# Kernel optimization log

Measured on AMD Instinct MI355X. Metric: run time of the kernel, lower is better.

Reference implementation:

```python
import jax, jax.numpy as jnp
import numpy as np

SCALE = float(1 << 15)
PREEMPH = 0.97
FRAME_LEN = 400
FRAME_SHIFT = 160
FFT_SIZE = 512
N_RFFT = FFT_SIZE // 2 + 1  # 257
EPS = float(np.finfo(np.float32).eps)


def _mel_scale(f):
    return 1127.0 * np.log(1.0 + f / 700.0)


def _get_mel_banks(num_bins=80, window_length_padded=512, sample_freq=16000.0,
                   low_freq=20.0, high_freq=0.0):
    # Kaldi-style triangular mel banks (vtln_warp=1.0 -> no warp)
    num_fft_bins = window_length_padded // 2  # 256
    nyquist = 0.5 * sample_freq
    if high_freq <= 0.0:
        high_freq = nyquist + high_freq  # 8000.0
    fft_bin_width = sample_freq / window_length_padded
    mel_low = _mel_scale(low_freq)
    mel_high = _mel_scale(high_freq)
    mel_delta = (mel_high - mel_low) / (num_bins + 1)
    bins = np.arange(num_bins, dtype=np.float64)[:, None]
    left = mel_low + bins * mel_delta
    center = left + mel_delta
    right = center + mel_delta
    mel_freqs = _mel_scale(fft_bin_width * np.arange(num_fft_bins, dtype=np.float64))[None, :]
    up = (mel_freqs - left) / (center - left)
    down = (right - mel_freqs) / (right - center)
    banks = np.maximum(0.0, np.minimum(up, down))  # [80, 256]
    return banks.astype(np.float32)


def _buffers():
    # Hamming window, periodic=False: 0.54 - 0.46*cos(2*pi*n/(N-1))
    n = np.arange(FRAME_LEN, dtype=np.float64)
    window = (0.54 - 0.46 * np.cos(2.0 * np.pi * n / (FRAME_LEN - 1))).astype(np.float32)
    mel = _get_mel_banks()  # [80, 256]
    mel_padded = np.pad(mel, ((0, 0), (0, 1)))  # pad one zero column -> [80, 257]
    mel_filters = mel_padded.T.copy()  # [257, 80]
    k = np.arange(N_RFFT, dtype=np.float64)
    t = np.arange(FFT_SIZE, dtype=np.float64)
    angles = 2.0 * np.pi * k[:, None] * t[None, :] / FFT_SIZE
    dft_cos = np.cos(angles).astype(np.float32)  # [257, 512]
    dft_sin = np.sin(angles).astype(np.float32)  # [257, 512]
    return window, mel_filters, dft_cos, dft_sin


def setup_inputs() -> dict:
    key = jax.random.key(0)
    waveforms = jax.random.normal(key, (32, 1, 480000), dtype=jnp.float32)
    window, mel_filters, dft_cos, dft_sin = _buffers()
    return {
        "waveforms": waveforms,
        "window": jnp.asarray(window),
        "mel_filters": jnp.asarray(mel_filters),
        "dft_cos": jnp.asarray(dft_cos),
        "dft_sin": jnp.asarray(dft_sin),
    }


def reference(waveforms, window, mel_filters, dft_cos, dft_sin):
    signal = waveforms[:, 0, :] * SCALE  # [B, T]
    T = signal.shape[-1]
    n_frames = (T - FRAME_LEN) // FRAME_SHIFT + 1
    # strided framing (equivalent to conv1d with identity kernel, stride=160)
    idx = jnp.arange(n_frames)[:, None] * FRAME_SHIFT + jnp.arange(FRAME_LEN)[None, :]
    frames = signal[:, idx]  # [B, F, 400]
    frames = frames - jnp.mean(frames, axis=2, keepdims=True)
    # pre-emphasis with replicate-padded previous sample
    prev = jnp.concatenate([frames[..., :1], frames[..., :-1]], axis=-1)
    frames = (frames - PREEMPH * prev) * window  # windowing fused
    frames = jnp.pad(frames, ((0, 0), (0, 0), (0, FFT_SIZE - FRAME_LEN)))  # [B, F, 512]
    real = jnp.matmul(frames, dft_cos.T)  # [B, F, 257]
    imag = jnp.matmul(frames, dft_sin.T)
    spectrum = real * real + imag * imag  # power spectrum
    mel = jnp.matmul(spectrum, mel_filters)  # [B, F, 80]
    mel = jnp.log(jnp.maximum(mel, EPS))
    return mel - jnp.mean(mel, axis=1, keepdims=True)
```

## Files before the change

kernel.cpp:

```cpp
#include <hip/hip_runtime.h>

#define BATCH     32
#define T_SAMP    480000
#define NFRAMES   2998
#define KLEN      400
#define KF        256
#define NMEL      80
#define EPS_F     1.1920928955078125e-07f
#define SCALE2    1073741824.0f
#define SPLIT_S   2048.0f
#define SPLIT_INV 4.8828125e-4f
#define MTE       132
#define NPART     16

typedef _Float16 f16x8 __attribute__((ext_vector_type(8)));
typedef float    f32x4 __attribute__((ext_vector_type(4)));

__global__ __launch_bounds__(256) void FbankWrapper_14285061226526_kernel(float* mpart)
{
    int i = blockIdx.x * 256 + threadIdx.x;
    if (i < NPART * BATCH * NMEL) mpart[i] = 0.f;
}

__global__ __launch_bounds__(256) void k_prep(const float* __restrict__ melf,
                                              const float* __restrict__ dcos,
                                              const float* __restrict__ dsin,
                                              int* __restrict__ loE, int* __restrict__ hiE,
                                              int* __restrict__ loO, int* __restrict__ hiO,
                                              float* __restrict__ melfTe,
                                              float* __restrict__ melfTo,
                                              _Float16* __restrict__ Bhe, _Float16* __restrict__ Ble,
                                              _Float16* __restrict__ Bho, _Float16* __restrict__ Blo)
{
    const int bid = blockIdx.x;
    const int tid = threadIdx.x;

    if (bid < 80) {
        __shared__ int sE0, sE1, sO0, sO1;
        if (tid == 0) { sE0 = 999; sE1 = 0; sO0 = 999; sO1 = 0; }
        __syncthreads();
        const int m = bid;
        if (tid < 129) {
            int bin = (tid == 0) ? 0 : (tid == 128) ? 256 : 2 * tid;
            float w = melf[(size_t)bin * NMEL + m];
            melfTe[(size_t)m * MTE + tid] = w;
            if (w > 0.f) { atomicMin(&sE0, tid); atomicMax(&sE1, tid + 1); }
        }
        if (tid < 128) {
            float w = melf[(size_t)(2 * tid + 1) * NMEL + m];
            melfTo[(size_t)m * MTE + tid] = w;
            if (w > 0.f) { atomicMin(&sO0, tid); atomicMax(&sO1, tid + 1); }
        }
        if (tid == 0) {
            melfTe[(size_t)m * MTE + 129] = 0.f;
            melfTe[(size_t)m * MTE + 130] = 0.f;
            melfTe[(size_t)m * MTE + 131] = 0.f;
            melfTo[(size_t)m * MTE + 128] = 0.f;
            melfTo[(size_t)m * MTE + 129] = 0.f;
            melfTo[(size_t)m * MTE + 130] = 0.f;
            melfTo[(size_t)m * MTE + 131] = 0.f;
        }
        __syncthreads();
        if (tid == 0) { loE[m] = sE0; hiE[m] = sE1; loO[m] = sO0; hiO[m] = sO1; }
        return;
    }

    int id = (bid - 80) * 256 + tid;
    if (id >= 16384) return;
    int g  = id >> 13;
    int r  = id & 8191;
    int ch = r >> 8;
    int c  = r & 255;
    int k  = ch * 8;
    int bin; int sn;
    if (g == 0) { bin = (c == 0) ? 0 : (c == 1) ? 256 : 2 * (c >> 1); sn = (c >= 2) && (c & 1); }
    else        { bin = 2 * (c >> 1) + 1;                             sn = c & 1; }
    const float* src = (sn ? dsin : dcos) + (size_t)bin * 512 + k;
    f16x8 hv, lv;
    #pragma unroll
    for (int j = 0; j < 8; ++j) {
        float v = src[j];
        _Float16 h = (_Float16)v;
        hv[j] = h;
        lv[j] = (_Float16)((v - (float)h) * SPLIT_S);
    }
    size_t off = ((size_t)ch * 256 + c) * 8;
    *(f16x8*)((g ? Bho : Bhe) + off) = hv;
    *(f16x8*)((g ? Blo : Ble) + off) = lv;
}

__device__ inline void y8_compute(const float* __restrict__ sig,
                                  const float* __restrict__ window,
                                  int k0, float mean, float ys[8])
{
    float4 x0 = *(const float4*)(sig + k0);
    float4 x1 = *(const float4*)(sig + k0 + 4);
    float4 w0 = *(const float4*)(window + k0);
    float4 w1 = *(const float4*)(window + k0 + 4);
    float xm1 = (k0 > 0) ? sig[k0 - 1] : x0.x;
    float xs[8] = {x0.x, x0.y, x0.z, x0.w, x1.x, x1.y, x1.z, x1.w};
    float wv[8] = {w0.x, w0.y, w0.z, w0.w, w1.x, w1.y, w1.z, w1.w};
    #pragma unroll
    for (int j = 0; j < 8; ++j) {
        float xp = (j == 0) ? xm1 : xs[j - 1];
        ys[j] = (xs[j] - 0.97f * xp - 0.03f * mean) * wv[j];
    }
}

__device__ inline void split_store(_Float16* dh, _Float16* dl, const float ys[8])
{
    f16x8 hv, lv;
    #pragma unroll
    for (int j = 0; j < 8; ++j) {
        _Float16 h = (_Float16)ys[j];
        hv[j] = h;
        lv[j] = (_Float16)((ys[j] - (float)h) * SPLIT_S);
    }
    *(f16x8*)dh = hv;
    *(f16x8*)dl = lv;
}

__global__ __launch_bounds__(512, 4) void k_main_pre(const float* __restrict__ wav,
                                                     const float* __restrict__ window,
                                                     const float* __restrict__ melfTe,
                                                     const float* __restrict__ melfTo,
                                                     const int* __restrict__ loE,
                                                     const int* __restrict__ hiE,
                                                     const int* __restrict__ loO,
                                                     const int* __restrict__ hiO,
                                                     const _Float16* __restrict__ Bhe,
                                                     const _Float16* __restrict__ Ble,
                                                     const _Float16* __restrict__ Bho,
                                                     const _Float16* __restrict__ Blo,
                                                     float* __restrict__ out,
                                                     float* __restrict__ mpart)
{
    __shared__ __align__(16) _Float16 Aeh[32][264];
    __shared__ __align__(16) _Float16 Ael[32][264];
    __shared__ __align__(16) _Float16 Aoh[32][168];
    __shared__ __align__(16) _Float16 Aol[32][168];
    __shared__ __align__(16) float    Sp[32][132];

    const int tid  = threadIdx.x;
    const int lane = tid & 63;
    const int wid  = tid >> 6;
    const int tile = blockIdx.x;

    {
        int fr = tid >> 4, og = tid & 15;
        int fb = tile * 32 + fr;
        int b  = fb / NFRAMES;
        int f  = fb - b * NFRAMES;
        const float* sig = wav + (size_t)b * T_SAMP + (size_t)f * 160;

        float s = 0.f;
        #pragma unroll
        for (int i = 0; i < 4; ++i) {
            int k0 = og * 8 + 128 * i;
            if (k0 < KLEN) {
                float4 x0 = *(const float4*)(sig + k0);
                float4 x1 = *(const float4*)(sig + k0 + 4);
                s += x0.x + x0.y + x0.z + x0.w + x1.x + x1.y + x1.z + x1.w;
            }
        }
        s += __shfl_xor(s, 1);
        s += __shfl_xor(s, 2);
        s += __shfl_xor(s, 4);
        s += __shfl_xor(s, 8);
        float mean = s * (1.0f / (float)KLEN);

        #pragma unroll
        for (int t2 = 0; t2 < 2; ++t2) {
            int c  = og + 16 * t2;
            int k0 = c * 8;
            float ys[8];
            y8_compute(sig, window, k0, mean, ys);
            if (c < 18) {
                float yb[8], ye[8], yo[8];
                y8_compute(sig, window, k0 + 256, mean, yb);
                #pragma unroll
                for (int j = 0; j < 8; ++j) { ye[j] = ys[j] + yb[j]; yo[j] = ys[j] - yb[j]; }
                split_store(&Aeh[fr][k0], &Ael[fr][k0], ye);
                split_store(&Aoh[fr][k0], &Aol[fr][k0], yo);
            } else {
                split_store(&Aeh[fr][k0], &Ael[fr][k0], ys);
                if (k0 < 160)
                    split_store(&Aoh[fr][k0], &Aol[fr][k0], ys);
            }
        }
    }
    __syncthreads();

    const int q  = lane >> 4, lr = lane & 15;
    const int mf = tid & 31;
    const int mg = tid >> 5;

    float accm[5];
    #pragma unroll
    for (int t = 0; t < 5; ++t) accm[t] = 0.f;

    #pragma unroll
    for (int p = 0; p < 2; ++p) {
        f32x4 aM[2][2], aC[2][2];
        #pragma unroll
        for (int mt = 0; mt < 2; ++mt)
            #pragma unroll
            for (int nt = 0; nt < 2; ++nt) {
                aM[mt][nt] = (f32x4){0.f, 0.f, 0.f, 0.f};
                aC[mt][nt] = (f32x4){0.f, 0.f, 0.f, 0.f};
            }

        const _Float16* Bh_ = p ? Bho : Bhe;
        const _Float16* Bl_ = p ? Blo : Ble;
        const _Float16* bph[2];
        const _Float16* blp[2];
        #pragma unroll
        for (int nt = 0; nt < 2; ++nt) {
            int c = wid * 32 + nt * 16 + lr;
            size_t off = (size_t)q * 2048 + (size_t)c * 8;
            bph[nt] = Bh_ + off;
            blp[nt] = Bl_ + off;
        }

        #pragma unroll
        for (int s = 0; s < 8; ++s) {
            const int kk = s * 32;
            f16x8 ah[2], al[2], bh[2], bl[2];
            if (p == 0 || s >= 5) {
                #pragma unroll
                for (int mt = 0; mt < 2; ++mt) {
                    ah[mt] = *(const f16x8*)&Aeh[mt * 16 + lr][kk + q * 8];
                    al[mt] = *(const f16x8*)&Ael[mt * 16 + lr][kk + q * 8];
                }
            } else {
                #pragma unroll
                for (int mt = 0; mt < 2; ++mt) {
                    ah[mt] = *(const f16x8*)&Aoh[mt * 16 + lr][kk + q * 8];
                    al[mt] = *(const f16x8*)&Aol[mt * 16 + lr][kk + q * 8];
                }
            }
            #pragma unroll
            for (int nt = 0; nt < 2; ++nt) {
                bh[nt] = *(const f16x8*)(bph[nt] + (size_t)s * 8192);
                bl[nt] = *(const f16x8*)(blp[nt] + (size_t)s * 8192);
            }
            #pragma unroll
            for (int mt = 0; mt < 2; ++mt)
                #pragma unroll
                for (int nt = 0; nt < 2; ++nt)
                    aM[mt][nt] = __builtin_amdgcn_mfma_f32_16x16x32_f16(
                        ah[mt], bh[nt], aM[mt][nt], 0, 0, 0);
            #pragma unroll
            for (int mt = 0; mt < 2; ++mt)
                #pragma unroll
                for (int nt = 0; nt < 2; ++nt)
                    aC[mt][nt] = __builtin_amdgcn_mfma_f32_16x16x32_f16(
                        al[mt], bh[nt], aC[mt][nt], 0, 0, 0);
            #pragma unroll
            for (int mt = 0; mt < 2; ++mt)
                #pragma unroll
                for (int nt = 0; nt < 2; ++nt)
                    aC[mt][nt] = __builtin_amdgcn_mfma_f32_16x16x32_f16(
                        ah[mt], bl[nt], aC[mt][nt], 0, 0, 0);
        }

        __syncthreads();
        #pragma unroll
        for (int mt = 0; mt < 2; ++mt)
            #pragma unroll
            for (int nt = 0; nt < 2; ++nt)
                #pragma unroll
                for (int r = 0; r < 4; ++r) {
                    float v = aM[mt][nt][r] + aC[mt][nt][r] * SPLIT_INV;
                    float o = __shfl_xor(v, 1);
                    int row = mt * 16 + q * 4 + r;
                    if (p == 0 && wid == 0 && nt == 0 && lr < 2) {
                        if (lr == 0) Sp[row][0] = v * v;
                    } else if ((lane & 1) == 0) {
                        int slot = (wid * 32 + nt * 16 + lr) >> 1;
                        Sp[row][slot] = v * v + o * o;
                    }
                }
        __syncthreads();

        const float* mfT = p ? melfTo : melfTe;
        const int*   loP = p ? loO : loE;
        const int*   hiP = p ? hiO : hiE;
        #pragma unroll
        for (int t = 0; t < 5; ++t) {
            int m  = mg + 16 * t;
            int ks = loP[m], ke = hiP[m];
            const float* wrow = mfT + (size_t)m * MTE;
            for (int k4 = ks & ~3; k4 < ke; k4 += 4) {
                f32x4  sv = *(const f32x4*)&Sp[mf][k4];
                float4 wv = *(const float4*)(wrow + k4);
                accm[t] += sv[0] * wv.x + sv[1] * wv.y + sv[2] * wv.z + sv[3] * wv.w;
            }
        }
    }

    {
        int fb = tile * 32 + mf;
        int b  = fb / NFRAMES;
        int b0 = (tile * 32) / NFRAMES;
        int bL = (tile * 32 + 31) / NFRAMES;
        size_t row = (size_t)fb;
        float* mp = mpart + (size_t)(tile & (NPART - 1)) * (BATCH * NMEL);
        float lg[5];
        #pragma unroll
        for (int t = 0; t < 5; ++t) {
            lg[t] = logf(fmaxf(accm[t] * SCALE2, EPS_F));
            out[row * NMEL + mg + 16 * t] = lg[t];
        }
        if (bL == b0) {
            #pragma unroll
            for (int t = 0; t < 5; ++t) {
                float v = lg[t];
                #pragma unroll
                for (int d = 1; d < 32; d <<= 1) v += __shfl_xor(v, d);
                if (mf == 0)
                    atomicAdd(&mp[b0 * NMEL + mg + 16 * t], v);
            }
        } else {
            #pragma unroll
            for (int t = 0; t < 5; ++t) {
                float v0 = (b == b0) ? lg[t] : 0.f;
                float v1 = lg[t] - v0;
                #pragma unroll
                for (int d = 1; d < 32; d <<= 1) {
                    v0 += __shfl_xor(v0, d);
                    v1 += __shfl_xor(v1, d);
                }
                if (mf == 0) {
                    atomicAdd(&mp[b0 * NMEL + mg + 16 * t], v0);
                    atomicAdd(&mp[bL * NMEL + mg + 16 * t], v1);
                }
            }
        }
    }
}

__global__ __launch_bounds__(256) void k_red(const float* __restrict__ mpart,
                                             float* __restrict__ means)
{
    int i = blockIdx.x * 256 + threadIdx.x;
    if (i < BATCH * NMEL) {
        float s = 0.f;
        #pragma unroll
        for (int p = 0; p < NPART; ++p) s += mpart[(size_t)p * BATCH * NMEL + i];
        means[i] = s;
    }
}

__global__ __launch_bounds__(256) void k_norm(const float* __restrict__ means,
                                              float* __restrict__ out)
{
    const int PER = NFRAMES * NMEL;
    int b = blockIdx.y;
    int e = blockIdx.x * 256 + threadIdx.x;
    if (e < PER) {
        int m = e % NMEL;
        size_t idx = (size_t)b * PER + e;
        out[idx] = out[idx] - means[b * NMEL + m] * (1.0f / (float)NFRAMES);
    }
}

extern "C" void kernel_launch(void* const* d_in, const int* in_sizes, int n_in,
                              void* d_out, int out_size, void* d_ws, size_t ws_size,
                              hipStream_t stream)
{
    const float* wav    = (const float*)d_in[0];
    const float* window = (const float*)d_in[1];
    const float* melf   = (const float*)d_in[2];
    const float* dcos   = (const float*)d_in[3];
    const float* dsin   = (const float*)d_in[4];
    float* out = (float*)d_out;

    char* ws = (char*)d_ws;
    float*     means  = (float*)ws;
    int*       loE    = (int*)(ws + 10240);
    int*       hiE    = (int*)(ws + 10560);
    int*       loO    = (int*)(ws + 10880);
    int*       hiO    = (int*)(ws + 11200);
    float*     melfTe = (float*)(ws + 11520);
    float*     melfTo = (float*)(ws + 53760);
    _Float16*  Bhe    = (_Float16*)(ws + 96256);
    _Float16*  Ble    = (_Float16*)(ws + 227328);
    _Float16*  Bho    = (_Float16*)(ws + 358400);
    _Float16*  Blo    = (_Float16*)(ws + 489472);
    float*     mpart  = (float*)(ws + 620544);

    FbankWrapper_14285061226526_kernel<<<160, 256, 0, stream>>>(mpart);
    k_prep<<<144, 256, 0, stream>>>(melf, dcos, dsin, loE, hiE, loO, hiO,
                                    melfTe, melfTo, Bhe, Ble, Bho, Blo);
    k_main_pre<<<2998, 512, 0, stream>>>(wav, window, melfTe, melfTo,
                                         loE, hiE, loO, hiO,
                                         Bhe, Ble, Bho, Blo, out, mpart);
    k_red<<<10, 256, 0, stream>>>(mpart, means);
    k_norm<<<dim3((NFRAMES * NMEL + 255) / 256, BATCH), 256, 0, stream>>>(means, out);
}
```

Measured before the change: 251.0 us.

## Fuse mean reduction into normalization kernel and raise MFMA wave priority

```diff
diff --git a/kernel.cpp b/kernel.cpp
--- a/kernel.cpp
+++ b/kernel.cpp
@@ -244,6 +244,7 @@
                 bh[nt] = *(const f16x8*)(bph[nt] + (size_t)s * 8192);
                 bl[nt] = *(const f16x8*)(blp[nt] + (size_t)s * 8192);
             }
+            __builtin_amdgcn_s_setprio(1);
             #pragma unroll
             for (int mt = 0; mt < 2; ++mt)
                 #pragma unroll
@@ -262,6 +263,7 @@
                 for (int nt = 0; nt < 2; ++nt)
                     aC[mt][nt] = __builtin_amdgcn_mfma_f32_16x16x32_f16(
                         ah[mt], bl[nt], aC[mt][nt], 0, 0, 0);
+            __builtin_amdgcn_s_setprio(0);
         }
 
         __syncthreads();
@@ -340,28 +342,30 @@
     }
 }
 
-__global__ __launch_bounds__(256) void k_red(const float* __restrict__ mpart,
-                                             float* __restrict__ means)
-{
-    int i = blockIdx.x * 256 + threadIdx.x;
-    if (i < BATCH * NMEL) {
+__global__ __launch_bounds__(256) void k_norm(const float* __restrict__ mpart,
+                                              float* __restrict__ out)
+{
+    __shared__ float lmean[NMEL];
+    const int PER = NFRAMES * NMEL;
+    const int b   = blockIdx.y;
+    const int tid = threadIdx.x;
+    if (tid < NMEL) {
         float s = 0.f;
         #pragma unroll
-        for (int p = 0; p < NPART; ++p) s += mpart[(size_t)p * BATCH * NMEL + i];
-        means[i] = s;
-    }
-}
-
-__global__ __launch_bounds__(256) void k_norm(const float* __restrict__ means,
-                                              float* __restrict__ out)
-{
-    const int PER = NFRAMES * NMEL;
-    int b = blockIdx.y;
-    int e = blockIdx.x * 256 + threadIdx.x;
-    if (e < PER) {
-        int m = e % NMEL;
-        size_t idx = (size_t)b * PER + e;
-        out[idx] = out[idx] - means[b * NMEL + m] * (1.0f / (float)NFRAMES);
+        for (int p = 0; p < NPART; ++p)
+            s += mpart[(size_t)p * (BATCH * NMEL) + b * NMEL + tid];
+        lmean[tid] = s * (1.0f / (float)NFRAMES);
+    }
+    __syncthreads();
+    int e0 = blockIdx.x * 1024 + tid;
+    #pragma unroll
+    for (int j = 0; j < 4; ++j) {
+        int e = e0 + j * 256;
+        if (e < PER) {
+            int m = e % NMEL;
+            size_t idx = (size_t)b * PER + e;
+            out[idx] = out[idx] - lmean[m];
+        }
     }
 }
 
@@ -377,7 +381,6 @@
     float* out = (float*)d_out;
 
     char* ws = (char*)d_ws;
-    float*     means  = (float*)ws;
     int*       loE    = (int*)(ws + 10240);
     int*       hiE    = (int*)(ws + 10560);
     int*       loO    = (int*)(ws + 10880);
@@ -396,6 +399,5 @@
     k_main_pre<<<2998, 512, 0, stream>>>(wav, window, melfTe, melfTo,
                                          loE, hiE, loO, hiO,
                                          Bhe, Ble, Bho, Blo, out, mpart);
-    k_red<<<10, 256, 0, stream>>>(mpart, means);
-    k_norm<<<dim3((NFRAMES * NMEL + 255) / 256, BATCH), 256, 0, stream>>>(means, out);
-}
+    k_norm<<<dim3((NFRAMES * NMEL + 1023) / 1024, BATCH), 256, 0, stream>>>(mpart, out);
+}
```

Measured after the change: 255.2 us. About the same (+1.7%).
